# Performance work log

Measured on AMD Instinct MI355X. Metric: run time of the kernel, lower is better.

## Reference

```python
import jax, jax.numpy as jnp
import numpy as np

LN_EPS = 1e-5
N_NODES = 100000
N_EDGES = 600000
HIDDEN = 128


def setup_inputs() -> dict:
    key = jax.random.key(0)
    ks = jax.random.split(key, 6)
    s = 1.0 / np.sqrt(HIDDEN)
    x = jax.random.normal(ks[0], (N_NODES, HIDDEN), dtype=jnp.float32)
    edge_index = jax.random.randint(ks[1], (2, N_EDGES), 0, N_NODES, dtype=jnp.int64)
    W1 = jax.random.normal(ks[2], (HIDDEN, HIDDEN), dtype=jnp.float32) * s
    b1 = jnp.zeros((HIDDEN,), dtype=jnp.float32)
    W2 = jax.random.normal(ks[3], (HIDDEN, HIDDEN), dtype=jnp.float32) * s
    b2 = jnp.zeros((HIDDEN,), dtype=jnp.float32)
    gamma = jnp.ones((HIDDEN,), dtype=jnp.float32)
    beta = jnp.zeros((HIDDEN,), dtype=jnp.float32)
    return {"x": x, "edge_index": edge_index, "W1": W1, "b1": b1,
            "W2": W2, "b2": b2, "gamma": gamma, "beta": beta}


def layer_norm(h, gamma, beta):
    mu = jnp.mean(h, axis=-1, keepdims=True)
    var = jnp.mean(jnp.square(h - mu), axis=-1, keepdims=True)
    return (h - mu) * jax.lax.rsqrt(var + LN_EPS) * gamma + beta


def reference(x, edge_index, W1, b1, W2, b2, gamma, beta):
    src, dst = edge_index[0], edge_index[1]
    # GIN aggregation (eps=0): (1+eps)*x + sum_{j in N(i)} x_j
    agg = x + jax.ops.segment_sum(x[src], dst, num_segments=x.shape[0])
    # MLP: Linear -> ReLU -> Linear
    h = jax.nn.relu(agg @ W1.T + b1) @ W2.T + b2
    h = jax.nn.relu(layer_norm(h, gamma, beta))
    # dropout is identity in eval mode
    return x + h
```

## Files before the change

kernel.cpp:

```cpp
#include <hip/hip_runtime.h>

#define H 128
#define LN_EPS 1e-5f
#define CAP 32

typedef __attribute__((ext_vector_type(8))) short bf16x8;
typedef __attribute__((ext_vector_type(4))) float f32x4;
typedef __attribute__((ext_vector_type(8))) unsigned short u16x8;

static __device__ __forceinline__ unsigned short f2bf(float f) {
  unsigned int u = __float_as_uint(f);
  u += 0x7fffu + ((u >> 16) & 1u);
  return (unsigned short)(u >> 16);
}

static __device__ __forceinline__ unsigned int cvt_pk_bf16(float lo, float hi) {
  unsigned int r;
  asm("v_cvt_pk_bf16_f32 %0, %1, %2" : "=v"(r) : "v"(lo), "v"(hi));
  return r;
}

static __device__ __forceinline__ void nt_st_f4(float* p, f32x4 v) {
  __builtin_nontemporal_store(v, (f32x4*)p);
}

static __device__ __forceinline__ void acc_bf8(float* a8, const uint4 v) {
  a8[0] += __uint_as_float(v.x << 16);
  a8[1] += __uint_as_float(v.x & 0xffff0000u);
  a8[2] += __uint_as_float(v.y << 16);
  a8[3] += __uint_as_float(v.y & 0xffff0000u);
  a8[4] += __uint_as_float(v.z << 16);
  a8[5] += __uint_as_float(v.z & 0xffff0000u);
  a8[6] += __uint_as_float(v.w << 16);
  a8[7] += __uint_as_float(v.w & 0xffff0000u);
}

template <int NT>
__device__ __forceinline__ void stage_w(const float* __restrict__ W,
                                        unsigned short* lds, int tid) {
#pragma unroll
  for (int it = 0; it < 4096 / NT; it++) {
    int i = tid + it * NT;
    int o = i >> 5;
    int k = (i & 31) << 2;
    float4 w = ((const float4*)W)[i];
    int byte = (o << 8) + (k << 1);
    byte ^= (o & 7) << 4;
    ushort4 wb;
    wb.x = f2bf(w.x); wb.y = f2bf(w.y); wb.z = f2bf(w.z); wb.w = f2bf(w.w);
    *(ushort4*)((char*)lds + byte) = wb;
  }
}

__global__ __launch_bounds__(256) void k_prep(
    const float* __restrict__ x, unsigned short* __restrict__ xb,
    const int* __restrict__ src, const int* __restrict__ dst,
    int* __restrict__ deg, int* __restrict__ slots, int ne, int nn) {
  const int t = blockIdx.x * 256 + threadIdx.x;
  const int nc = nn * 16;
  const bool do_cast = t < nc;
  const bool do_edge = t < ne;
  int d = 0, s = 0;
  if (do_edge) { d = dst[t]; s = src[t]; }
  float4 p, q;
  if (do_cast) {
    p = ((const float4*)x)[(size_t)t * 2];
    q = ((const float4*)x)[(size_t)t * 2 + 1];
  }
  if (do_cast) {
    u16x8 r;
    r[0] = f2bf(p.x); r[1] = f2bf(p.y); r[2] = f2bf(p.z); r[3] = f2bf(p.w);
    r[4] = f2bf(q.x); r[5] = f2bf(q.y); r[6] = f2bf(q.z); r[7] = f2bf(q.w);
    *(u16x8*)(xb + (size_t)t * 8) = r;
  }
  if (do_edge) {
    int pos = atomicAdd(&deg[d], 1);
    if (pos < CAP) slots[(size_t)pos * nn + d] = s;
  }
}

__global__ void k_fill_cm(const int* __restrict__ src, const int* __restrict__ dst,
                          int* __restrict__ deg, int* __restrict__ slots,
                          int ne, int nn) {
  int e = blockIdx.x * 256 + threadIdx.x;
  if (e >= ne) return;
  int d = dst[e];
  int p = atomicAdd(&deg[d], 1);
  if (p < CAP) slots[(size_t)p * nn + d] = src[e];
}

__global__ __launch_bounds__(512, 4) void k_mlp3b(
    const float* __restrict__ x, const unsigned short* __restrict__ xb,
    const int* __restrict__ deg, const int* __restrict__ slots,
    const float* __restrict__ W1, const float* __restrict__ b1,
    const float* __restrict__ W2, const float* __restrict__ b2,
    const float* __restrict__ gamma, const float* __restrict__ beta,
    float* __restrict__ out, int n_nodes) {
  __shared__ unsigned short Wlds[128 * 128];

  const int tid  = threadIdx.x;
  const int wave = tid >> 6;
  const int lane = tid & 63;
  const int l15  = lane & 15;
  const int lg   = lane >> 4;
  const int xorv = (l15 & 7) << 4;
  const int row_base = blockIdx.x * 128 + wave * 16;
  const bool active = row_base < n_nodes;

  stage_w<512>(W1, Wlds, tid);

  float a[4][8];
  float4 xres[8];
  if (active) {
    const int row = row_base + l15;
    const float* xr = x + (size_t)row * H + lg * 8;
#pragma unroll
    for (int ks = 0; ks < 4; ks++) {
      float4 p = *(const float4*)(xr + ks * 32);
      float4 q = *(const float4*)(xr + ks * 32 + 4);
      a[ks][0] = p.x; a[ks][1] = p.y; a[ks][2] = p.z; a[ks][3] = p.w;
      a[ks][4] = q.x; a[ks][5] = q.y; a[ks][6] = q.z; a[ks][7] = q.w;
    }
    const float* xrr = x + (size_t)row * H + lg * 4;
#pragma unroll
    for (int n = 0; n < 8; n++)
      xres[n] = *(const float4*)(xrr + n * 16);

    int d = deg[row];
    d = (d > CAP) ? CAP : d;
    const int* sl = slots + row;
    const int nn = n_nodes;
    const char* xbL = (const char*)xb + lg * 16;

    int sA = (0 < d) ? sl[0] : 0;
    int sB = (1 < d) ? sl[(size_t)1 * nn] : 0;
    int i = 0;
    for (; i + 2 <= d; i += 2) {
      const int sA2 = (i + 2 < d) ? sl[(size_t)(i + 2) * nn] : 0;
      const int sB2 = (i + 3 < d) ? sl[(size_t)(i + 3) * nn] : 0;
      const char* pA = xbL + (size_t)sA * 256;
      const char* pB = xbL + (size_t)sB * 256;
      uint4 va[4], vb[4];
#pragma unroll
      for (int ks = 0; ks < 4; ks++) {
        va[ks] = *(const uint4*)(pA + ks * 64);
        vb[ks] = *(const uint4*)(pB + ks * 64);
      }
#pragma unroll
      for (int ks = 0; ks < 4; ks++) {
        acc_bf8(a[ks], va[ks]);
        acc_bf8(a[ks], vb[ks]);
      }
      sA = sA2; sB = sB2;
    }
    if (i < d) {
      const char* pA = xbL + (size_t)sA * 256;
#pragma unroll
      for (int ks = 0; ks < 4; ks++) {
        uint4 v = *(const uint4*)(pA + ks * 64);
        acc_bf8(a[ks], v);
      }
    }
  }
  __syncthreads();

  unsigned int w0[8], w1[8];
  if (active) {
    bf16x8 af[4];
#pragma unroll
    for (int ks = 0; ks < 4; ks++)
#pragma unroll
      for (int j = 0; j < 8; j++) af[ks][j] = (short)f2bf(a[ks][j]);

    f32x4 acc1[8];
#pragma unroll
    for (int n = 0; n < 8; n++) acc1[n] = (f32x4){0.f, 0.f, 0.f, 0.f};
#pragma unroll
    for (int ks = 0; ks < 4; ks++) {
      const int k0 = ks * 32 + lg * 8;
#pragma unroll
      for (int n = 0; n < 8; n++) {
        const int o = n * 16 + l15;
        bf16x8 bf = *(const bf16x8*)((const char*)Wlds +
                     ((((o << 8) + (k0 << 1))) ^ xorv));
        acc1[n] = __builtin_amdgcn_mfma_f32_16x16x32_bf16(bf, af[ks], acc1[n], 0, 0, 0);
      }
    }
#pragma unroll
    for (int n = 0; n < 8; n++) {
      const float4 bb = *(const float4*)(b1 + n * 16 + lg * 4);
      float v0 = fmaxf(acc1[n][0] + bb.x, 0.f);
      float v1 = fmaxf(acc1[n][1] + bb.y, 0.f);
      float v2 = fmaxf(acc1[n][2] + bb.z, 0.f);
      float v3 = fmaxf(acc1[n][3] + bb.w, 0.f);
      w0[n] = cvt_pk_bf16(v0, v1);
      w1[n] = cvt_pk_bf16(v2, v3);
    }
  }
  __syncthreads();

  stage_w<512>(W2, Wlds, tid);

  bf16x8 a2f[4];
  if (active) {
    const int src_lo = ((lg & 1) << 5) + l15;
    const int src_hi = src_lo + 16;
    const bool nhi = (lg & 2) != 0;
#pragma unroll
    for (int ks = 0; ks < 4; ks++) {
      unsigned int m0a = __shfl(w0[2 * ks],     src_lo);
      unsigned int m0b = __shfl(w0[2 * ks + 1], src_lo);
      unsigned int m1a = __shfl(w1[2 * ks],     src_lo);
      unsigned int m1b = __shfl(w1[2 * ks + 1], src_lo);
      unsigned int m2a = __shfl(w0[2 * ks],     src_hi);
      unsigned int m2b = __shfl(w0[2 * ks + 1], src_hi);
      unsigned int m3a = __shfl(w1[2 * ks],     src_hi);
      unsigned int m3b = __shfl(w1[2 * ks + 1], src_hi);
      union { unsigned int u[4]; bf16x8 v; } c;
      c.u[0] = nhi ? m0b : m0a;
      c.u[1] = nhi ? m1b : m1a;
      c.u[2] = nhi ? m2b : m2a;
      c.u[3] = nhi ? m3b : m3a;
      a2f[ks] = c.v;
    }
  }
  __syncthreads();

  if (!active) return;

  f32x4 acc2[8];
#pragma unroll
  for (int n = 0; n < 8; n++) acc2[n] = (f32x4){0.f, 0.f, 0.f, 0.f};
#pragma unroll
  for (int ks = 0; ks < 4; ks++) {
    const int k0 = ks * 32 + lg * 8;
#pragma unroll
    for (int n = 0; n < 8; n++) {
      const int o = n * 16 + l15;
      bf16x8 bf = *(const bf16x8*)((const char*)Wlds +
                   ((((o << 8) + (k0 << 1))) ^ xorv));
      acc2[n] = __builtin_amdgcn_mfma_f32_16x16x32_bf16(bf, a2f[ks], acc2[n], 0, 0, 0);
    }
  }

  const int row = row_base + l15;
  float sum = 0.f, ssq = 0.f;
#pragma unroll
  for (int n = 0; n < 8; n++) {
    const float4 bb = *(const float4*)(b2 + n * 16 + lg * 4);
    acc2[n][0] += bb.x; acc2[n][1] += bb.y;
    acc2[n][2] += bb.z; acc2[n][3] += bb.w;
#pragma unroll
    for (int r = 0; r < 4; r++) {
      float v = acc2[n][r];
      sum += v;
      ssq += v * v;
    }
  }
  sum += __shfl_xor(sum, 16, 64);
  sum += __shfl_xor(sum, 32, 64);
  ssq += __shfl_xor(ssq, 16, 64);
  ssq += __shfl_xor(ssq, 32, 64);
  const float mu = sum * (1.0f / H);
  const float var = ssq * (1.0f / H) - mu * mu;
  const float rs = rsqrtf(var + LN_EPS);

#pragma unroll
  for (int n = 0; n < 8; n++) {
    const int col = n * 16 + lg * 4;
    const float4 g4  = *(const float4*)(gamma + col);
    const float4 be4 = *(const float4*)(beta + col);
    const float4 x4  = xres[n];
    f32x4 o4;
    o4.x = x4.x + fmaxf((acc2[n][0] - mu) * rs * g4.x + be4.x, 0.f);
    o4.y = x4.y + fmaxf((acc2[n][1] - mu) * rs * g4.y + be4.y, 0.f);
    o4.z = x4.z + fmaxf((acc2[n][2] - mu) * rs * g4.z + be4.z, 0.f);
    o4.w = x4.w + fmaxf((acc2[n][3] - mu) * rs * g4.w + be4.w, 0.f);
    nt_st_f4(out + (size_t)row * H + col, o4);
  }
}

__global__ __launch_bounds__(512, 4) void k_mlp3f(
    const float* __restrict__ x,
    const int* __restrict__ deg, const int* __restrict__ slots,
    const float* __restrict__ W1, const float* __restrict__ b1,
    const float* __restrict__ W2, const float* __restrict__ b2,
    const float* __restrict__ gamma, const float* __restrict__ beta,
    float* __restrict__ out, int n_nodes) {
  __shared__ unsigned short Wlds[128 * 128];

  const int tid  = threadIdx.x;
  const int wave = tid >> 6;
  const int lane = tid & 63;
  const int l15  = lane & 15;
  const int lg   = lane >> 4;
  const int xorv = (l15 & 7) << 4;
  const int row_base = blockIdx.x * 128 + wave * 16;
  const bool active = row_base < n_nodes;

  stage_w<512>(W1, Wlds, tid);

  float a[4][8];
  if (active) {
    const int row = row_base + l15;
    const float* xr = x + (size_t)row * H + lg * 8;
#pragma unroll
    for (int ks = 0; ks < 4; ks++) {
      float4 p = *(const float4*)(xr + ks * 32);
      float4 q = *(const float4*)(xr + ks * 32 + 4);
      a[ks][0] = p.x; a[ks][1] = p.y; a[ks][2] = p.z; a[ks][3] = p.w;
      a[ks][4] = q.x; a[ks][5] = q.y; a[ks][6] = q.z; a[ks][7] = q.w;
    }
    int d = deg[row];
    d = (d > CAP) ? CAP : d;
    const int* sl = slots + row;
    const int nn = n_nodes;

    int sA = (0 < d) ? sl[0] : 0;
    int sB = (1 < d) ? sl[(size_t)1 * nn] : 0;
    int i = 0;
    for (; i + 2 <= d; i += 2) {
      const int sA2 = (i + 2 < d) ? sl[(size_t)(i + 2) * nn] : 0;
      const int sB2 = (i + 3 < d) ? sl[(size_t)(i + 3) * nn] : 0;
      const float* xA = x + (size_t)sA * H + lg * 8;
      const float* xB = x + (size_t)sB * H + lg * 8;
      float4 pa[4], qa[4], pb[4], qb[4];
#pragma unroll
      for (int ks = 0; ks < 4; ks++) {
        pa[ks] = *(const float4*)(xA + ks * 32);
        qa[ks] = *(const float4*)(xA + ks * 32 + 4);
        pb[ks] = *(const float4*)(xB + ks * 32);
        qb[ks] = *(const float4*)(xB + ks * 32 + 4);
      }
#pragma unroll
      for (int ks = 0; ks < 4; ks++) {
        a[ks][0] += pa[ks].x + pb[ks].x;
        a[ks][1] += pa[ks].y + pb[ks].y;
        a[ks][2] += pa[ks].z + pb[ks].z;
        a[ks][3] += pa[ks].w + pb[ks].w;
        a[ks][4] += qa[ks].x + qb[ks].x;
        a[ks][5] += qa[ks].y + qb[ks].y;
        a[ks][6] += qa[ks].z + qb[ks].z;
        a[ks][7] += qa[ks].w + qb[ks].w;
      }
      sA = sA2; sB = sB2;
    }
    if (i < d) {
      const float* xA = x + (size_t)sA * H + lg * 8;
#pragma unroll
      for (int ks = 0; ks < 4; ks++) {
        float4 p = *(const float4*)(xA + ks * 32);
        float4 q = *(const float4*)(xA + ks * 32 + 4);
        a[ks][0] += p.x; a[ks][1] += p.y; a[ks][2] += p.z; a[ks][3] += p.w;
        a[ks][4] += q.x; a[ks][5] += q.y; a[ks][6] += q.z; a[ks][7] += q.w;
      }
    }
  }
  __syncthreads();

  unsigned int w0[8], w1[8];
  if (active) {
    bf16x8 af[4];
#pragma unroll
    for (int ks = 0; ks < 4; ks++)
#pragma unroll
      for (int j = 0; j < 8; j++) af[ks][j] = (short)f2bf(a[ks][j]);

    f32x4 acc1[8];
#pragma unroll
    for (int n = 0; n < 8; n++) acc1[n] = (f32x4){0.f, 0.f, 0.f, 0.f};
#pragma unroll
    for (int ks = 0; ks < 4; ks++) {
      const int k0 = ks * 32 + lg * 8;
#pragma unroll
      for (int n = 0; n < 8; n++) {
        const int o = n * 16 + l15;
        bf16x8 bf = *(const bf16x8*)((const char*)Wlds +
                     ((((o << 8) + (k0 << 1))) ^ xorv));
        acc1[n] = __builtin_amdgcn_mfma_f32_16x16x32_bf16(bf, af[ks], acc1[n], 0, 0, 0);
      }
    }
#pragma unroll
    for (int n = 0; n < 8; n++) {
      const float4 bb = *(const float4*)(b1 + n * 16 + lg * 4);
      float v0 = fmaxf(acc1[n][0] + bb.x, 0.f);
      float v1 = fmaxf(acc1[n][1] + bb.y, 0.f);
      float v2 = fmaxf(acc1[n][2] + bb.z, 0.f);
      float v3 = fmaxf(acc1[n][3] + bb.w, 0.f);
      w0[n] = cvt_pk_bf16(v0, v1);
      w1[n] = cvt_pk_bf16(v2, v3);
    }
  }
  __syncthreads();

  stage_w<512>(W2, Wlds, tid);

  bf16x8 a2f[4];
  if (active) {
    const int src_lo = ((lg & 1) << 5) + l15;
    const int src_hi = src_lo + 16;
    const bool nhi = (lg & 2) != 0;
#pragma unroll
    for (int ks = 0; ks < 4; ks++) {
      unsigned int m0a = __shfl(w0[2 * ks],     src_lo);
      unsigned int m0b = __shfl(w0[2 * ks + 1], src_lo);
      unsigned int m1a = __shfl(w1[2 * ks],     src_lo);
      unsigned int m1b = __shfl(w1[2 * ks + 1], src_lo);
      unsigned int m2a = __shfl(w0[2 * ks],     src_hi);
      unsigned int m2b = __shfl(w0[2 * ks + 1], src_hi);
      unsigned int m3a = __shfl(w1[2 * ks],     src_hi);
      unsigned int m3b = __shfl(w1[2 * ks + 1], src_hi);
      union { unsigned int u[4]; bf16x8 v; } c;
      c.u[0] = nhi ? m0b : m0a;
      c.u[1] = nhi ? m1b : m1a;
      c.u[2] = nhi ? m2b : m2a;
      c.u[3] = nhi ? m3b : m3a;
      a2f[ks] = c.v;
    }
  }
  __syncthreads();

  if (!active) return;

  f32x4 acc2[8];
#pragma unroll
  for (int n = 0; n < 8; n++) acc2[n] = (f32x4){0.f, 0.f, 0.f, 0.f};
#pragma unroll
  for (int ks = 0; ks < 4; ks++) {
    const int k0 = ks * 32 + lg * 8;
#pragma unroll
    for (int n = 0; n < 8; n++) {
      const int o = n * 16 + l15;
      bf16x8 bf = *(const bf16x8*)((const char*)Wlds +
                   ((((o << 8) + (k0 << 1))) ^ xorv));
      acc2[n] = __builtin_amdgcn_mfma_f32_16x16x32_bf16(bf, a2f[ks], acc2[n], 0, 0, 0);
    }
  }

  const int row = row_base + l15;
  float sum = 0.f, ssq = 0.f;
#pragma unroll
  for (int n = 0; n < 8; n++) {
    const float4 bb = *(const float4*)(b2 + n * 16 + lg * 4);
    acc2[n][0] += bb.x; acc2[n][1] += bb.y;
    acc2[n][2] += bb.z; acc2[n][3] += bb.w;
#pragma unroll
    for (int r = 0; r < 4; r++) {
      float v = acc2[n][r];
      sum += v;
      ssq += v * v;
    }
  }
  sum += __shfl_xor(sum, 16, 64);
  sum += __shfl_xor(sum, 32, 64);
  ssq += __shfl_xor(ssq, 16, 64);
  ssq += __shfl_xor(ssq, 32, 64);
  const float mu = sum * (1.0f / H);
  const float var = ssq * (1.0f / H) - mu * mu;
  const float rs = rsqrtf(var + LN_EPS);

#pragma unroll
  for (int n = 0; n < 8; n++) {
    const int col = n * 16 + lg * 4;
    const float4 g4  = *(const float4*)(gamma + col);
    const float4 be4 = *(const float4*)(beta + col);
    const float4 x4  = *(const float4*)(x + (size_t)row * H + col);
    float4 o4;
    o4.x = x4.x + fmaxf((acc2[n][0] - mu) * rs * g4.x + be4.x, 0.f);
    o4.y = x4.y + fmaxf((acc2[n][1] - mu) * rs * g4.y + be4.y, 0.f);
    o4.z = x4.z + fmaxf((acc2[n][2] - mu) * rs * g4.z + be4.z, 0.f);
    o4.w = x4.w + fmaxf((acc2[n][3] - mu) * rs * g4.w + be4.w, 0.f);
    *(float4*)(out + (size_t)row * H + col) = o4;
  }
}

extern "C" void kernel_launch(void* const* d_in, const int* in_sizes, int n_in,
                              void* d_out, int out_size, void* d_ws, size_t ws_size,
                              hipStream_t stream) {
  const float* x  = (const float*)d_in[0];
  const int*   ei = (const int*)d_in[1];
  const float* W1 = (const float*)d_in[2];
  const float* b1 = (const float*)d_in[3];
  const float* W2 = (const float*)d_in[4];
  const float* b2 = (const float*)d_in[5];
  const float* gm = (const float*)d_in[6];
  const float* bt = (const float*)d_in[7];
  float* out = (float*)d_out;

  const int n_nodes = in_sizes[0] / H;
  const int n_edges = in_sizes[1] / 2;
  const int* src = ei;
  const int* dst = ei + n_edges;

  const size_t slots_off = ((size_t)n_nodes + 63) & ~(size_t)63;
  const size_t xb_off    = slots_off + (size_t)CAP * n_nodes;
  const size_t need_bf   = (xb_off + (size_t)n_nodes * 64) * sizeof(int);
  const size_t need_cm   = xb_off * sizeof(int);

  if (ws_size >= need_bf) {
    int* deg   = (int*)d_ws;
    int* slots = (int*)d_ws + slots_off;
    unsigned short* xb = (unsigned short*)((int*)d_ws + xb_off);

    hipMemsetAsync(deg, 0, (size_t)n_nodes * sizeof(int), stream);
    const int ncast = n_nodes * 16;
    const int work = (n_edges > ncast) ? n_edges : ncast;
    k_prep<<<(work + 255) / 256, 256, 0, stream>>>(
        x, xb, src, dst, deg, slots, n_edges, n_nodes);
    k_mlp3b<<<(n_nodes + 127) / 128, 512, 0, stream>>>(
        x, xb, deg, slots, W1, b1, W2, b2, gm, bt, out, n_nodes);
    return;
  }

  if (ws_size >= need_cm) {
    int* deg   = (int*)d_ws;
    int* slots = (int*)d_ws + slots_off;

    hipMemsetAsync(deg, 0, (size_t)n_nodes * sizeof(int), stream);
    k_fill_cm<<<(n_edges + 255) / 256, 256, 0, stream>>>(
        src, dst, deg, slots, n_edges, n_nodes);
    k_mlp3f<<<(n_nodes + 127) / 128, 512, 0, stream>>>(
        x, deg, slots, W1, b1, W2, b2, gm, bt, out, n_nodes);
    return;
  }
}
```

Measured before the change: 127.1 us.

## Halve fused MLP block size and unroll neighbor gather by three

The fused gather+MLP kernel now runs 256-thread blocks covering 64 rows instead of 512 threads covering 128 rows, with launch bounds raised to 5 blocks per CU. The neighbor aggregation loop is unrolled to three edges per iteration with prefetched slot indices, and a tail handles up to two leftover edges. The aim is more memory-level parallelism in the random bf16 row gathers and finer-grained scheduling. The cost is that W1 and W2 are staged into LDS twice as often per row, and the extra in-flight loads raise register pressure.

New measurement: 153.1 us. 20.4% more time.

```diff
diff --git a/kernel.cpp b/kernel.cpp
--- a/kernel.cpp
+++ b/kernel.cpp
@@ -89,7 +89,7 @@
   if (p < CAP) slots[(size_t)p * nn + d] = src[e];
 }
 
-__global__ __launch_bounds__(512, 4) void k_mlp3b(
+__global__ __launch_bounds__(256, 5) void k_mlp3b(
     const float* __restrict__ x, const unsigned short* __restrict__ xb,
     const int* __restrict__ deg, const int* __restrict__ slots,
     const float* __restrict__ W1, const float* __restrict__ b1,
@@ -104,10 +104,10 @@
   const int l15  = lane & 15;
   const int lg   = lane >> 4;
   const int xorv = (l15 & 7) << 4;
-  const int row_base = blockIdx.x * 128 + wave * 16;
+  const int row_base = blockIdx.x * 64 + wave * 16;
   const bool active = row_base < n_nodes;
 
-  stage_w<512>(W1, Wlds, tid);
+  stage_w<256>(W1, Wlds, tid);
 
   float a[4][8];
   float4 xres[8];
@@ -132,33 +132,50 @@
     const int nn = n_nodes;
     const char* xbL = (const char*)xb + lg * 16;
 
-    int sA = (0 < d) ? sl[0] : 0;
-    int sB = (1 < d) ? sl[(size_t)1 * nn] : 0;
+    int s0 = (0 < d) ? sl[0] : 0;
+    int s1 = (1 < d) ? sl[(size_t)1 * nn] : 0;
+    int s2 = (2 < d) ? sl[(size_t)2 * nn] : 0;
     int i = 0;
-    for (; i + 2 <= d; i += 2) {
-      const int sA2 = (i + 2 < d) ? sl[(size_t)(i + 2) * nn] : 0;
-      const int sB2 = (i + 3 < d) ? sl[(size_t)(i + 3) * nn] : 0;
-      const char* pA = xbL + (size_t)sA * 256;
-      const char* pB = xbL + (size_t)sB * 256;
-      uint4 va[4], vb[4];
+    for (; i + 3 <= d; i += 3) {
+      const int t0 = (i + 3 < d) ? sl[(size_t)(i + 3) * nn] : 0;
+      const int t1 = (i + 4 < d) ? sl[(size_t)(i + 4) * nn] : 0;
+      const int t2 = (i + 5 < d) ? sl[(size_t)(i + 5) * nn] : 0;
+      const char* pA = xbL + (size_t)s0 * 256;
+      const char* pB = xbL + (size_t)s1 * 256;
+      const char* pC = xbL + (size_t)s2 * 256;
+      uint4 va[4], vb[4], vc[4];
 #pragma unroll
       for (int ks = 0; ks < 4; ks++) {
         va[ks] = *(const uint4*)(pA + ks * 64);
         vb[ks] = *(const uint4*)(pB + ks * 64);
+        vc[ks] = *(const uint4*)(pC + ks * 64);
       }
 #pragma unroll
       for (int ks = 0; ks < 4; ks++) {
         acc_bf8(a[ks], va[ks]);
         acc_bf8(a[ks], vb[ks]);
-      }
-      sA = sA2; sB = sB2;
+        acc_bf8(a[ks], vc[ks]);
+      }
+      s0 = t0; s1 = t1; s2 = t2;
     }
     if (i < d) {
-      const char* pA = xbL + (size_t)sA * 256;
-#pragma unroll
-      for (int ks = 0; ks < 4; ks++) {
-        uint4 v = *(const uint4*)(pA + ks * 64);
-        acc_bf8(a[ks], v);
+      const char* pA = xbL + (size_t)s0 * 256;
+      uint4 va[4];
+#pragma unroll
+      for (int ks = 0; ks < 4; ks++) va[ks] = *(const uint4*)(pA + ks * 64);
+      if (i + 1 < d) {
+        const char* pB = xbL + (size_t)s1 * 256;
+        uint4 vb[4];
+#pragma unroll
+        for (int ks = 0; ks < 4; ks++) vb[ks] = *(const uint4*)(pB + ks * 64);
+#pragma unroll
+        for (int ks = 0; ks < 4; ks++) {
+          acc_bf8(a[ks], va[ks]);
+          acc_bf8(a[ks], vb[ks]);
+        }
+      } else {
+#pragma unroll
+        for (int ks = 0; ks < 4; ks++) acc_bf8(a[ks], va[ks]);
       }
     }
   }
@@ -199,7 +216,7 @@
   }
   __syncthreads();
 
-  stage_w<512>(W2, Wlds, tid);
+  stage_w<256>(W2, Wlds, tid);
 
   bf16x8 a2f[4];
   if (active) {
@@ -507,7 +524,7 @@
     const int work = (n_edges > ncast) ? n_edges : ncast;
     k_prep<<<(work + 255) / 256, 256, 0, stream>>>(
         x, xb, src, dst, deg, slots, n_edges, n_nodes);
-    k_mlp3b<<<(n_nodes + 127) / 128, 512, 0, stream>>>(
+    k_mlp3b<<<(n_nodes + 63) / 64, 256, 0, stream>>>(
         x, xb, deg, slots, W1, b1, W2, b2, gm, bt, out, n_nodes);
     return;
   }
```
